# Optimization experiments

Measured on AMD Instinct MI355X. Metric: run time of the kernel, lower is better.

The kernel has to match this reference:

```python
import jax, jax.numpy as jnp
import numpy as np

HID = 512

def setup_inputs() -> dict:
    key = jax.random.key(0)
    k1, k2, k3, k4, k5, k6 = jax.random.split(key, 6)
    B, T, H = 32, 4096, HID
    enc_seq = jax.random.normal(k1, (B, T, H), dtype=jnp.float32)
    enc_mask = jax.random.randint(k2, (B, T), 0, 2, dtype=jnp.int32)
    dec_state = jax.random.normal(k3, (B, H), dtype=jnp.float32)
    # Linear weights, torch layout: y = x @ W.T
    scale = 1.0 / np.sqrt(H)
    W_h = jax.random.uniform(k4, (H, H), jnp.float32, -scale, scale)
    W_s = jax.random.uniform(k5, (H, H), jnp.float32, -scale, scale)
    v = jax.random.uniform(k6, (H,), jnp.float32, -scale, scale)
    return {"enc_seq": enc_seq, "enc_mask": enc_mask, "dec_state": dec_state,
            "W_h": W_h, "W_s": W_s, "v": v}

def reference(enc_seq, enc_mask, dec_state, W_h, W_s, v):
    # s: [B,H] -> [B,1,H] broadcast over T; h: [B,T,H]
    s = jnp.einsum('bh,kh->bk', dec_state, W_s)[:, None, :]
    h = jnp.einsum('bth,kh->btk', enc_seq, W_h)
    e = jnp.einsum('bth,h->bt', jnp.tanh(h + s), v)  # [B,T]
    e = jnp.where(enc_mask == 0, jnp.float32(-1e9), e)
    a = jax.nn.softmax(e, axis=1)  # [B,T]
    ctx = jnp.einsum('bt,bth->bh', a, enc_seq)  # [B,H]
    return (ctx, a)
```

## Files before the change

kernel.cpp:

```cpp
#include <hip/hip_runtime.h>
#include <hip/hip_bf16.h>
#include <cstdint>
#include <cstddef>

#define HID 512
#define T_SZ 4096

typedef __bf16 bf16x8 __attribute__((ext_vector_type(8)));
typedef float f32x4 __attribute__((ext_vector_type(4)));

__device__ __forceinline__ unsigned short f2bf_rne(float f) {
    unsigned int u = __float_as_uint(f);
    unsigned int r = (u + 0x7FFFu + ((u >> 16) & 1u)) >> 16;
    return (unsigned short)r;
}

__device__ __forceinline__ bf16x8 pack8(float4 x0, float4 x1) {
    bf16x8 r;
    r[0] = (__bf16)x0.x; r[1] = (__bf16)x0.y; r[2] = (__bf16)x0.z; r[3] = (__bf16)x0.w;
    r[4] = (__bf16)x1.x; r[5] = (__bf16)x1.y; r[6] = (__bf16)x1.z; r[7] = (__bf16)x1.w;
    return r;
}

__device__ __forceinline__ float fast_tanh(float x) {
    float e = __expf(2.0f * x);
    return 1.0f - 2.0f / (e + 1.0f);
}

__device__ __forceinline__ void gload_lds16(const void* g, void* l) {
    __builtin_amdgcn_global_load_lds(
        (const __attribute__((address_space(1))) unsigned int*)g,
        (__attribute__((address_space(3))) unsigned int*)l, 16, 0, 0);
}

__global__ void k_s(const float* __restrict__ dec, const float* __restrict__ Ws,
                    float* __restrict__ s) {
    int idx = blockIdx.x * 256 + threadIdx.x;
    int b = idx >> 9, n = idx & 511;
    const float4* dp = reinterpret_cast<const float4*>(dec + (size_t)b * HID);
    const float4* wp = reinterpret_cast<const float4*>(Ws + (size_t)n * HID);
    float acc = 0.f;
#pragma unroll 8
    for (int i = 0; i < HID / 4; ++i) {
        float4 d = dp[i], w = wp[i];
        acc += d.x * w.x + d.y * w.y + d.z * w.z + d.w * w.w;
    }
    s[idx] = acc;
}

__global__ void k_pack(const float* __restrict__ Wh, uint4* __restrict__ Wb) {
    int idx = blockIdx.x * 256 + threadIdx.x;
    int n = idx >> 6;
    int k0 = (idx & 63) * 8;
    const float4* p = reinterpret_cast<const float4*>(Wh + (size_t)n * HID + k0);
    float4 x0 = p[0], x1 = p[1];
    uint4 w;
    w.x = f2bf_rne(x0.x) | ((unsigned)f2bf_rne(x0.y) << 16);
    w.y = f2bf_rne(x0.z) | ((unsigned)f2bf_rne(x0.w) << 16);
    w.z = f2bf_rne(x1.x) | ((unsigned)f2bf_rne(x1.y) << 16);
    w.w = f2bf_rne(x1.z) | ((unsigned)f2bf_rne(x1.w) << 16);
    int n4g = n >> 4, c = n & 15, kk = k0 >> 5, g = (k0 >> 3) & 3;
    Wb[(size_t)kk * 2048 + n4g * 64 + g * 16 + c] = w;
}

__global__ void __launch_bounds__(256, 3) k_gemm_e(
    const float* __restrict__ enc, const uint4* __restrict__ Wb,
    const float* __restrict__ s, const float* __restrict__ v,
    float* __restrict__ part_e) {
    __shared__ __align__(16) unsigned char Abuf[2][4096];
    __shared__ __align__(16) unsigned char Bbuf[2][16384];
    __shared__ float red[4][64];

    const int tid = threadIdx.x;
    const int p = blockIdx.x;
    const int logical = (p & 7) * 512 + (p >> 3);
    const int h = logical & 1;
    const size_t row0 = (size_t)(logical >> 1) * 64;
    const int b = (int)(row0 >> 12);

    const int lane = tid & 63, wid = tid >> 6;
    const int c = lane & 15, g4 = lane >> 4;

    float sv_s[4], sv_v[4];
#pragma unroll
    for (int ni = 0; ni < 4; ++ni) {
        int n = h * 256 + wid * 64 + ni * 16 + c;
        sv_s[ni] = s[b * HID + n];
        sv_v[ni] = v[n];
    }

    const int ar = tid >> 2;
    const int ak = (tid & 3) * 8;
    const float* Ag = enc + (row0 + ar) * HID + ak;
    const int abyte = ar * 64 + (tid & 3) * 16;
    const uint4* Bg = Wb + h * 1024;
    const int wchunk = wid * 64;

    float4 a0 = *reinterpret_cast<const float4*>(Ag);
    float4 a1 = *reinterpret_cast<const float4*>(Ag + 4);
#pragma unroll
    for (int i = 0; i < 4; ++i)
        gload_lds16(Bg + (wchunk + i * 256) + (lane), &Bbuf[0][(wchunk + i * 256) * 16]);
    *reinterpret_cast<bf16x8*>(&Abuf[0][abyte]) = pack8(a0, a1);
    a0 = *reinterpret_cast<const float4*>(Ag + 32);
    a1 = *reinterpret_cast<const float4*>(Ag + 36);
    __syncthreads();

    f32x4 acc[4][4] = {};

    for (int kk = 0; kk < 16; ++kk) {
        const int cur = kk & 1, nxt = cur ^ 1;
        if (kk < 15) {
#pragma unroll
            for (int i = 0; i < 4; ++i)
                gload_lds16(Bg + (size_t)(kk + 1) * 2048 + (wchunk + i * 256) + lane,
                            &Bbuf[nxt][(wchunk + i * 256) * 16]);
            *reinterpret_cast<bf16x8*>(&Abuf[nxt][abyte]) = pack8(a0, a1);
        }
        if (kk < 14) {
            a0 = *reinterpret_cast<const float4*>(Ag + (kk + 2) * 32);
            a1 = *reinterpret_cast<const float4*>(Ag + (kk + 2) * 32 + 4);
        }
        bf16x8 af[4], bfr[4];
#pragma unroll
        for (int mi = 0; mi < 4; ++mi)
            af[mi] = *reinterpret_cast<const bf16x8*>(&Abuf[cur][(mi * 16 + c) * 64 + g4 * 16]);
#pragma unroll
        for (int ni = 0; ni < 4; ++ni)
            bfr[ni] = *reinterpret_cast<const bf16x8*>(&Bbuf[cur][((wid * 4 + ni) * 64 + lane) * 16]);
#pragma unroll
        for (int mi = 0; mi < 4; ++mi)
#pragma unroll
            for (int ni = 0; ni < 4; ++ni)
                acc[mi][ni] = __builtin_amdgcn_mfma_f32_16x16x32_bf16(
                    af[mi], bfr[ni], acc[mi][ni], 0, 0, 0);
        __syncthreads();
    }

    float e_part[4][4] = {};
#pragma unroll
    for (int ni = 0; ni < 4; ++ni)
#pragma unroll
        for (int mi = 0; mi < 4; ++mi)
#pragma unroll
            for (int r = 0; r < 4; ++r)
                e_part[mi][r] += fast_tanh(acc[mi][ni][r] + sv_s[ni]) * sv_v[ni];

#pragma unroll
    for (int m = 1; m <= 8; m <<= 1)
#pragma unroll
        for (int mi = 0; mi < 4; ++mi)
#pragma unroll
            for (int r = 0; r < 4; ++r)
                e_part[mi][r] += __shfl_xor(e_part[mi][r], m);

    if (c == 0) {
#pragma unroll
        for (int mi = 0; mi < 4; ++mi)
#pragma unroll
            for (int r = 0; r < 4; ++r)
                red[wid][mi * 16 + g4 * 4 + r] = e_part[mi][r];
    }
    __syncthreads();
    if (tid < 64)
        part_e[(size_t)h * 131072 + row0 + tid] =
            red[0][tid] + red[1][tid] + red[2][tid] + red[3][tid];
}

__global__ void k_softmax(const float* __restrict__ part_e, float* __restrict__ a,
                          const int* __restrict__ mask) {
    int b = blockIdx.x, tid = threadIdx.x;
    int lane = tid & 63, wid = tid >> 6;
    __shared__ float red[16];
    float vals[4]; int ms[4];
    float mx = -1e30f;
#pragma unroll
    for (int j = 0; j < 4; ++j) {
        size_t t = (size_t)b * T_SZ + tid + j * 1024;
        vals[j] = part_e[t] + part_e[131072 + t];
        ms[j] = mask[t];
        if (ms[j]) mx = fmaxf(mx, vals[j]);
    }
#pragma unroll
    for (int m = 32; m >= 1; m >>= 1) mx = fmaxf(mx, __shfl_xor(mx, m));
    if (lane == 0) red[wid] = mx;
    __syncthreads();
    if (tid == 0) {
        float m2 = red[0];
        for (int i = 1; i < 16; ++i) m2 = fmaxf(m2, red[i]);
        red[0] = m2;
    }
    __syncthreads();
    mx = red[0];
    __syncthreads();
    float pv[4]; float sum = 0.f;
#pragma unroll
    for (int j = 0; j < 4; ++j) { pv[j] = ms[j] ? __expf(vals[j] - mx) : 0.f; sum += pv[j]; }
#pragma unroll
    for (int m = 32; m >= 1; m >>= 1) sum += __shfl_xor(sum, m);
    if (lane == 0) red[wid] = sum;
    __syncthreads();
    if (tid == 0) {
        float s2 = 0.f;
        for (int i = 0; i < 16; ++i) s2 += red[i];
        red[0] = s2;
    }
    __syncthreads();
    float inv = 1.f / red[0];
#pragma unroll
    for (int j = 0; j < 4; ++j)
        a[(size_t)b * T_SZ + tid + j * 1024] = pv[j] * inv;
}

__global__ void k_ctx(const float* __restrict__ enc, const float* __restrict__ a,
                      float2* __restrict__ part) {
    int ts = blockIdx.x, b = blockIdx.y, tid = threadIdx.x;
    size_t rbase = (size_t)b * T_SZ + (size_t)ts * 128;
    const float2* ep = reinterpret_cast<const float2*>(enc + rbase * HID) + tid;
    const float* ap = a + rbase;
    float ax = 0.f, ay = 0.f, bx = 0.f, by = 0.f;
#pragma unroll 2
    for (int t = 0; t < 128; t += 2) {
        float a0 = ap[t], a1 = ap[t + 1];
        float2 e0 = ep[(size_t)t * 256], e1 = ep[(size_t)(t + 1) * 256];
        ax += a0 * e0.x; ay += a0 * e0.y;
        bx += a1 * e1.x; by += a1 * e1.y;
    }
    float2 r; r.x = ax + bx; r.y = ay + by;
    part[(size_t)(b * 32 + ts) * 256 + tid] = r;
}

__global__ void k_ctxred(const float* __restrict__ part, float* __restrict__ ctx) {
    int idx = blockIdx.x * 256 + threadIdx.x;
    int b = idx >> 9, h = idx & 511;
    float sum = 0.f;
#pragma unroll
    for (int ts = 0; ts < 32; ++ts) sum += part[(size_t)(b * 32 + ts) * 512 + h];
    ctx[idx] = sum;
}

extern "C" void kernel_launch(void* const* d_in, const int* in_sizes, int n_in,
                              void* d_out, int out_size, void* d_ws, size_t ws_size,
                              hipStream_t stream) {
    const float* enc  = (const float*)d_in[0];
    const int*   mask = (const int*)d_in[1];
    const float* dec  = (const float*)d_in[2];
    const float* Wh   = (const float*)d_in[3];
    const float* Ws   = (const float*)d_in[4];
    const float* v    = (const float*)d_in[5];

    float* out = (float*)d_out;
    float* ctx = out;
    float* a   = out + 16384;

    float* ws     = (float*)d_ws;
    float* s      = ws;
    uint4* Wb     = (uint4*)(ws + 16384);
    float* part_e = ws + 16384 + 131072;
    float* part   = part_e + 262144;

    hipLaunchKernelGGL(k_s,      dim3(64),      dim3(256),  0, stream, dec, Ws, s);
    hipLaunchKernelGGL(k_pack,   dim3(128),     dim3(256),  0, stream, Wh, Wb);
    hipLaunchKernelGGL(k_gemm_e, dim3(4096),    dim3(256),  0, stream, enc, Wb, s, v, part_e);
    hipLaunchKernelGGL(k_softmax,dim3(32),      dim3(1024), 0, stream, part_e, a, mask);
    hipLaunchKernelGGL(k_ctx,    dim3(32, 32),  dim3(256),  0, stream, enc, a, (float2*)part);
    hipLaunchKernelGGL(k_ctxred, dim3(64),      dim3(256),  0, stream, part, ctx);
}
```

Baseline: 192.0 us.

## Enlarge GEMM tile to 128x256 with 2x2 warp grid and triple-buffered LDS

The fused score GEMM now processes 128 rows per block instead of 64, using a 2x2 wave layout where each wave computes 64x128. This halves the number of blocks and the redundant reloading of the packed W_h tiles per row. It also adds a three-stage LDS pipeline with explicit vmcnt waits and barriers so global loads run two k-steps ahead. The cost is higher register and LDS use, which drops the occupancy target from 3 to 2 blocks per CU, and the hand-written waitcnt sequencing is more fragile.

```diff
diff --git a/kernel.cpp b/kernel.cpp
--- a/kernel.cpp
+++ b/kernel.cpp
@@ -59,100 +59,124 @@
     w.y = f2bf_rne(x0.z) | ((unsigned)f2bf_rne(x0.w) << 16);
     w.z = f2bf_rne(x1.x) | ((unsigned)f2bf_rne(x1.y) << 16);
     w.w = f2bf_rne(x1.z) | ((unsigned)f2bf_rne(x1.w) << 16);
-    int n4g = n >> 4, c = n & 15, kk = k0 >> 5, g = (k0 >> 3) & 3;
-    Wb[(size_t)kk * 2048 + n4g * 64 + g * 16 + c] = w;
-}
-
-__global__ void __launch_bounds__(256, 3) k_gemm_e(
+    int n4 = n >> 4, c = n & 15, kk = k0 >> 5, g = (k0 >> 3) & 3;
+    Wb[(size_t)kk * 2048 + n4 * 64 + g * 16 + c] = w;
+}
+
+__global__ void __launch_bounds__(256, 2) k_gemm_e(
     const float* __restrict__ enc, const uint4* __restrict__ Wb,
     const float* __restrict__ s, const float* __restrict__ v,
     float* __restrict__ part_e) {
-    __shared__ __align__(16) unsigned char Abuf[2][4096];
-    __shared__ __align__(16) unsigned char Bbuf[2][16384];
+    __shared__ __align__(16) unsigned char Abuf[3][8192];
+    __shared__ __align__(16) unsigned char Bbuf[3][16384];
     __shared__ float red[4][64];
 
     const int tid = threadIdx.x;
     const int p = blockIdx.x;
-    const int logical = (p & 7) * 512 + (p >> 3);
+    const int logical = (p & 7) * 256 + (p >> 3);
     const int h = logical & 1;
-    const size_t row0 = (size_t)(logical >> 1) * 64;
+    const int m = logical >> 1;
+    const size_t row0 = (size_t)m * 128;
     const int b = (int)(row0 >> 12);
 
     const int lane = tid & 63, wid = tid >> 6;
     const int c = lane & 15, g4 = lane >> 4;
-
-    float sv_s[4], sv_v[4];
-#pragma unroll
-    for (int ni = 0; ni < 4; ++ni) {
-        int n = h * 256 + wid * 64 + ni * 16 + c;
+    const int wm = wid >> 1, wn = wid & 1;
+
+    float sv_s[8], sv_v[8];
+#pragma unroll
+    for (int ni = 0; ni < 8; ++ni) {
+        int n = h * 256 + wn * 128 + ni * 16 + c;
         sv_s[ni] = s[b * HID + n];
         sv_v[ni] = v[n];
     }
-
-    const int ar = tid >> 2;
-    const int ak = (tid & 3) * 8;
-    const float* Ag = enc + (row0 + ar) * HID + ak;
-    const int abyte = ar * 64 + (tid & 3) * 16;
-    const uint4* Bg = Wb + h * 1024;
-    const int wchunk = wid * 64;
-
-    float4 a0 = *reinterpret_cast<const float4*>(Ag);
-    float4 a1 = *reinterpret_cast<const float4*>(Ag + 4);
+    asm volatile("s_waitcnt vmcnt(0)" ::: "memory");
+
+    const int rt0 = tid >> 6, gg = (tid >> 4) & 3, cc = tid & 15;
+    const float* Ag0 = enc + (row0 + rt0 * 16 + cc) * HID + gg * 8;
+    const float* Ag1 = Ag0 + (size_t)64 * HID;
+    const uint4* Bg = Wb + h * 1024 + wid * 64 + lane;
+
+    float4 ar[2][4];
+
+#pragma unroll
+    for (int q = 0; q < 2; ++q)
+        ar[0][q * 2]     = *reinterpret_cast<const float4*>((q ? Ag1 : Ag0)),
+        ar[0][q * 2 + 1] = *reinterpret_cast<const float4*>((q ? Ag1 : Ag0) + 4);
 #pragma unroll
     for (int i = 0; i < 4; ++i)
-        gload_lds16(Bg + (wchunk + i * 256) + (lane), &Bbuf[0][(wchunk + i * 256) * 16]);
-    *reinterpret_cast<bf16x8*>(&Abuf[0][abyte]) = pack8(a0, a1);
-    a0 = *reinterpret_cast<const float4*>(Ag + 32);
-    a1 = *reinterpret_cast<const float4*>(Ag + 36);
-    __syncthreads();
-
-    f32x4 acc[4][4] = {};
-
+        gload_lds16(Bg + i * 256, &Bbuf[0][(i * 256 + wid * 64) * 16]);
+    asm volatile("" ::: "memory");
+#pragma unroll
+    for (int q = 0; q < 2; ++q)
+        ar[1][q * 2]     = *reinterpret_cast<const float4*>((q ? Ag1 : Ag0) + 32),
+        ar[1][q * 2 + 1] = *reinterpret_cast<const float4*>((q ? Ag1 : Ag0) + 36);
+#pragma unroll
+    for (int i = 0; i < 4; ++i)
+        gload_lds16(Bg + 2048 + i * 256, &Bbuf[1][(i * 256 + wid * 64) * 16]);
+    *reinterpret_cast<bf16x8*>(&Abuf[0][tid * 16])         = pack8(ar[0][0], ar[0][1]);
+    *reinterpret_cast<bf16x8*>(&Abuf[0][(tid + 256) * 16]) = pack8(ar[0][2], ar[0][3]);
+    asm volatile("s_waitcnt vmcnt(8) lgkmcnt(0)\n\ts_barrier" ::: "memory");
+
+    f32x4 acc[4][8] = {};
+
+#pragma unroll
     for (int kk = 0; kk < 16; ++kk) {
-        const int cur = kk & 1, nxt = cur ^ 1;
-        if (kk < 15) {
+        if (kk + 2 <= 15) {
+#pragma unroll
+            for (int q = 0; q < 2; ++q) {
+                const float* Agq = (q ? Ag1 : Ag0) + (kk + 2) * 32;
+                ar[kk & 1][q * 2]     = *reinterpret_cast<const float4*>(Agq);
+                ar[kk & 1][q * 2 + 1] = *reinterpret_cast<const float4*>(Agq + 4);
+            }
 #pragma unroll
             for (int i = 0; i < 4; ++i)
-                gload_lds16(Bg + (size_t)(kk + 1) * 2048 + (wchunk + i * 256) + lane,
-                            &Bbuf[nxt][(wchunk + i * 256) * 16]);
-            *reinterpret_cast<bf16x8*>(&Abuf[nxt][abyte]) = pack8(a0, a1);
+                gload_lds16(Bg + (size_t)(kk + 2) * 2048 + i * 256,
+                            &Bbuf[(kk + 2) % 3][(i * 256 + wid * 64) * 16]);
         }
-        if (kk < 14) {
-            a0 = *reinterpret_cast<const float4*>(Ag + (kk + 2) * 32);
-            a1 = *reinterpret_cast<const float4*>(Ag + (kk + 2) * 32 + 4);
+        if (kk + 1 <= 15) {
+            const int wb = (kk + 1) % 3, wp_ = (kk + 1) & 1;
+            *reinterpret_cast<bf16x8*>(&Abuf[wb][tid * 16])         = pack8(ar[wp_][0], ar[wp_][1]);
+            *reinterpret_cast<bf16x8*>(&Abuf[wb][(tid + 256) * 16]) = pack8(ar[wp_][2], ar[wp_][3]);
         }
-        bf16x8 af[4], bfr[4];
-#pragma unroll
-        for (int mi = 0; mi < 4; ++mi)
-            af[mi] = *reinterpret_cast<const bf16x8*>(&Abuf[cur][(mi * 16 + c) * 64 + g4 * 16]);
-#pragma unroll
-        for (int ni = 0; ni < 4; ++ni)
-            bfr[ni] = *reinterpret_cast<const bf16x8*>(&Bbuf[cur][((wid * 4 + ni) * 64 + lane) * 16]);
-#pragma unroll
-        for (int mi = 0; mi < 4; ++mi)
-#pragma unroll
-            for (int ni = 0; ni < 4; ++ni)
+        bf16x8 af[4], bfr[8];
+#pragma unroll
+        for (int mi = 0; mi < 4; ++mi)
+            af[mi] = *reinterpret_cast<const bf16x8*>(
+                &Abuf[kk % 3][((wm * 4 + mi) * 64 + lane) * 16]);
+#pragma unroll
+        for (int ni = 0; ni < 8; ++ni)
+            bfr[ni] = *reinterpret_cast<const bf16x8*>(
+                &Bbuf[kk % 3][((wn * 8 + ni) * 64 + lane) * 16]);
+#pragma unroll
+        for (int mi = 0; mi < 4; ++mi)
+#pragma unroll
+            for (int ni = 0; ni < 8; ++ni)
                 acc[mi][ni] = __builtin_amdgcn_mfma_f32_16x16x32_bf16(
                     af[mi], bfr[ni], acc[mi][ni], 0, 0, 0);
-        __syncthreads();
+        if (kk <= 13)
+            asm volatile("s_waitcnt vmcnt(8) lgkmcnt(0)\n\ts_barrier" ::: "memory");
+        else if (kk == 14)
+            asm volatile("s_waitcnt vmcnt(0) lgkmcnt(0)\n\ts_barrier" ::: "memory");
     }
 
     float e_part[4][4] = {};
 #pragma unroll
-    for (int ni = 0; ni < 4; ++ni)
+    for (int ni = 0; ni < 8; ++ni) {
+        float sn = sv_s[ni], vn = sv_v[ni];
 #pragma unroll
         for (int mi = 0; mi < 4; ++mi)
 #pragma unroll
             for (int r = 0; r < 4; ++r)
-                e_part[mi][r] += fast_tanh(acc[mi][ni][r] + sv_s[ni]) * sv_v[ni];
-
-#pragma unroll
-    for (int m = 1; m <= 8; m <<= 1)
+                e_part[mi][r] += fast_tanh(acc[mi][ni][r] + sn) * vn;
+    }
+#pragma unroll
+    for (int mm = 1; mm <= 8; mm <<= 1)
 #pragma unroll
         for (int mi = 0; mi < 4; ++mi)
 #pragma unroll
             for (int r = 0; r < 4; ++r)
-                e_part[mi][r] += __shfl_xor(e_part[mi][r], m);
+                e_part[mi][r] += __shfl_xor(e_part[mi][r], mm);
 
     if (c == 0) {
 #pragma unroll
@@ -162,9 +186,11 @@
                 red[wid][mi * 16 + g4 * 4 + r] = e_part[mi][r];
     }
     __syncthreads();
-    if (tid < 64)
+    if (tid < 128) {
+        int wm2 = tid >> 6, r = tid & 63;
         part_e[(size_t)h * 131072 + row0 + tid] =
-            red[0][tid] + red[1][tid] + red[2][tid] + red[3][tid];
+            red[wm2 * 2][r] + red[wm2 * 2 + 1][r];
+    }
 }
 
 __global__ void k_softmax(const float* __restrict__ part_e, float* __restrict__ a,
@@ -261,7 +287,7 @@
 
     hipLaunchKernelGGL(k_s,      dim3(64),      dim3(256),  0, stream, dec, Ws, s);
     hipLaunchKernelGGL(k_pack,   dim3(128),     dim3(256),  0, stream, Wh, Wb);
-    hipLaunchKernelGGL(k_gemm_e, dim3(4096),    dim3(256),  0, stream, enc, Wb, s, v, part_e);
+    hipLaunchKernelGGL(k_gemm_e, dim3(2048),    dim3(256),  0, stream, enc, Wb, s, v, part_e);
     hipLaunchKernelGGL(k_softmax,dim3(32),      dim3(1024), 0, stream, part_e, a, mask);
     hipLaunchKernelGGL(k_ctx,    dim3(32, 32),  dim3(256),  0, stream, enc, a, (float2*)part);
     hipLaunchKernelGGL(k_ctxred, dim3(64),      dim3(256),  0, stream, part, ctx);
```

Measured after the change: 206.1 us. +7.4%, slower.

## Split GEMM N into four quarters and load W_h fragments directly into registers

Applied to the files above, without the earlier changes.

The fused GEMM+tanh kernel now splits the 512 output columns into four 128-wide slices instead of two 256-wide ones, doubling the grid to 8192 blocks. Each wave now covers 32 columns, and the B (W_h) fragments are loaded straight from global memory into registers with double buffering, so the B LDS buffers and global_load_lds are gone. This cuts LDS use and raises the occupancy target to 4 blocks per CU. The cost is that each enc row tile is read and converted to bf16 twice as often, and softmax must now sum four partial-score buffers instead of two.

```diff
diff --git a/kernel.cpp b/kernel.cpp
--- a/kernel.cpp
+++ b/kernel.cpp
@@ -25,12 +25,6 @@
 __device__ __forceinline__ float fast_tanh(float x) {
     float e = __expf(2.0f * x);
     return 1.0f - 2.0f / (e + 1.0f);
-}
-
-__device__ __forceinline__ void gload_lds16(const void* g, void* l) {
-    __builtin_amdgcn_global_load_lds(
-        (const __attribute__((address_space(1))) unsigned int*)g,
-        (__attribute__((address_space(3))) unsigned int*)l, 16, 0, 0);
 }
 
 __global__ void k_s(const float* __restrict__ dec, const float* __restrict__ Ws,
@@ -59,100 +53,106 @@
     w.y = f2bf_rne(x0.z) | ((unsigned)f2bf_rne(x0.w) << 16);
     w.z = f2bf_rne(x1.x) | ((unsigned)f2bf_rne(x1.y) << 16);
     w.w = f2bf_rne(x1.z) | ((unsigned)f2bf_rne(x1.w) << 16);
-    int n4g = n >> 4, c = n & 15, kk = k0 >> 5, g = (k0 >> 3) & 3;
-    Wb[(size_t)kk * 2048 + n4g * 64 + g * 16 + c] = w;
-}
-
-__global__ void __launch_bounds__(256, 3) k_gemm_e(
+    int n4 = n >> 4, c = n & 15, kk = k0 >> 5, g = (k0 >> 3) & 3;
+    Wb[(size_t)kk * 2048 + n4 * 64 + g * 16 + c] = w;
+}
+
+__global__ void __launch_bounds__(256, 4) k_gemm_e(
     const float* __restrict__ enc, const uint4* __restrict__ Wb,
     const float* __restrict__ s, const float* __restrict__ v,
     float* __restrict__ part_e) {
     __shared__ __align__(16) unsigned char Abuf[2][4096];
-    __shared__ __align__(16) unsigned char Bbuf[2][16384];
     __shared__ float red[4][64];
 
     const int tid = threadIdx.x;
     const int p = blockIdx.x;
-    const int logical = (p & 7) * 512 + (p >> 3);
-    const int h = logical & 1;
-    const size_t row0 = (size_t)(logical >> 1) * 64;
+    const int logical = (p & 7) * 1024 + (p >> 3);
+    const int h = logical & 3;
+    const int m = logical >> 2;
+    const size_t row0 = (size_t)m * 64;
     const int b = (int)(row0 >> 12);
 
     const int lane = tid & 63, wid = tid >> 6;
     const int c = lane & 15, g4 = lane >> 4;
 
-    float sv_s[4], sv_v[4];
-#pragma unroll
-    for (int ni = 0; ni < 4; ++ni) {
-        int n = h * 256 + wid * 64 + ni * 16 + c;
+    float sv_s[2], sv_v[2];
+#pragma unroll
+    for (int ni = 0; ni < 2; ++ni) {
+        int n = h * 128 + wid * 32 + ni * 16 + c;
         sv_s[ni] = s[b * HID + n];
         sv_v[ni] = v[n];
     }
 
-    const int ar = tid >> 2;
-    const int ak = (tid & 3) * 8;
-    const float* Ag = enc + (row0 + ar) * HID + ak;
-    const int abyte = ar * 64 + (tid & 3) * 16;
-    const uint4* Bg = Wb + h * 1024;
-    const int wchunk = wid * 64;
-
-    float4 a0 = *reinterpret_cast<const float4*>(Ag);
-    float4 a1 = *reinterpret_cast<const float4*>(Ag + 4);
-#pragma unroll
-    for (int i = 0; i < 4; ++i)
-        gload_lds16(Bg + (wchunk + i * 256) + (lane), &Bbuf[0][(wchunk + i * 256) * 16]);
-    *reinterpret_cast<bf16x8*>(&Abuf[0][abyte]) = pack8(a0, a1);
-    a0 = *reinterpret_cast<const float4*>(Ag + 32);
-    a1 = *reinterpret_cast<const float4*>(Ag + 36);
-    __syncthreads();
-
-    f32x4 acc[4][4] = {};
-
+    const int arow = ((tid >> 6) << 4) + (tid & 15);
+    const int ag = (tid >> 4) & 3;
+    const float* Ag = enc + (row0 + arow) * HID + ag * 8;
+    const int abyte = tid * 16;
+    const uint4* Bg = Wb + (h * 8 + wid * 2) * 64 + lane;
+
+    float4 aR[2][2];
+    uint4  bR[2][2];
+
+    {
+        float4 x0 = *reinterpret_cast<const float4*>(Ag);
+        float4 x1 = *reinterpret_cast<const float4*>(Ag + 4);
+        bR[0][0] = Bg[0];
+        bR[0][1] = Bg[64];
+        bR[1][0] = Bg[2048];
+        bR[1][1] = Bg[2048 + 64];
+        *reinterpret_cast<bf16x8*>(&Abuf[0][abyte]) = pack8(x0, x1);
+        aR[1][0] = *reinterpret_cast<const float4*>(Ag + 32);
+        aR[1][1] = *reinterpret_cast<const float4*>(Ag + 36);
+    }
+    asm volatile("s_waitcnt lgkmcnt(0)\n\ts_barrier" ::: "memory");
+
+    f32x4 acc[4][2] = {};
+
+#pragma unroll
     for (int kk = 0; kk < 16; ++kk) {
-        const int cur = kk & 1, nxt = cur ^ 1;
-        if (kk < 15) {
-#pragma unroll
-            for (int i = 0; i < 4; ++i)
-                gload_lds16(Bg + (size_t)(kk + 1) * 2048 + (wchunk + i * 256) + lane,
-                            &Bbuf[nxt][(wchunk + i * 256) * 16]);
-            *reinterpret_cast<bf16x8*>(&Abuf[nxt][abyte]) = pack8(a0, a1);
+        if (kk + 2 <= 15) {
+            aR[kk & 1][0] = *reinterpret_cast<const float4*>(Ag + (kk + 2) * 32);
+            aR[kk & 1][1] = *reinterpret_cast<const float4*>(Ag + (kk + 2) * 32 + 4);
         }
-        if (kk < 14) {
-            a0 = *reinterpret_cast<const float4*>(Ag + (kk + 2) * 32);
-            a1 = *reinterpret_cast<const float4*>(Ag + (kk + 2) * 32 + 4);
+        if (kk + 1 <= 15)
+            *reinterpret_cast<bf16x8*>(&Abuf[(kk + 1) & 1][abyte]) =
+                pack8(aR[(kk + 1) & 1][0], aR[(kk + 1) & 1][1]);
+        bf16x8 af[4];
+#pragma unroll
+        for (int mi = 0; mi < 4; ++mi)
+            af[mi] = *reinterpret_cast<const bf16x8*>(
+                &Abuf[kk & 1][(mi * 64 + lane) * 16]);
+#pragma unroll
+        for (int mi = 0; mi < 4; ++mi)
+#pragma unroll
+            for (int ni = 0; ni < 2; ++ni)
+                acc[mi][ni] = __builtin_amdgcn_mfma_f32_16x16x32_bf16(
+                    af[mi], *reinterpret_cast<bf16x8*>(&bR[kk & 1][ni]),
+                    acc[mi][ni], 0, 0, 0);
+        if (kk + 2 <= 15) {
+            bR[kk & 1][0] = Bg[(size_t)(kk + 2) * 2048];
+            bR[kk & 1][1] = Bg[(size_t)(kk + 2) * 2048 + 64];
         }
-        bf16x8 af[4], bfr[4];
-#pragma unroll
-        for (int mi = 0; mi < 4; ++mi)
-            af[mi] = *reinterpret_cast<const bf16x8*>(&Abuf[cur][(mi * 16 + c) * 64 + g4 * 16]);
-#pragma unroll
-        for (int ni = 0; ni < 4; ++ni)
-            bfr[ni] = *reinterpret_cast<const bf16x8*>(&Bbuf[cur][((wid * 4 + ni) * 64 + lane) * 16]);
-#pragma unroll
-        for (int mi = 0; mi < 4; ++mi)
-#pragma unroll
-            for (int ni = 0; ni < 4; ++ni)
-                acc[mi][ni] = __builtin_amdgcn_mfma_f32_16x16x32_bf16(
-                    af[mi], bfr[ni], acc[mi][ni], 0, 0, 0);
-        __syncthreads();
+        if (kk < 15)
+            asm volatile("s_waitcnt lgkmcnt(0)\n\ts_barrier" ::: "memory");
     }
 
     float e_part[4][4] = {};
 #pragma unroll
-    for (int ni = 0; ni < 4; ++ni)
+    for (int ni = 0; ni < 2; ++ni) {
+        float sn = sv_s[ni], vn = sv_v[ni];
 #pragma unroll
         for (int mi = 0; mi < 4; ++mi)
 #pragma unroll
             for (int r = 0; r < 4; ++r)
-                e_part[mi][r] += fast_tanh(acc[mi][ni][r] + sv_s[ni]) * sv_v[ni];
-
-#pragma unroll
-    for (int m = 1; m <= 8; m <<= 1)
+                e_part[mi][r] += fast_tanh(acc[mi][ni][r] + sn) * vn;
+    }
+#pragma unroll
+    for (int mm = 1; mm <= 8; mm <<= 1)
 #pragma unroll
         for (int mi = 0; mi < 4; ++mi)
 #pragma unroll
             for (int r = 0; r < 4; ++r)
-                e_part[mi][r] += __shfl_xor(e_part[mi][r], m);
+                e_part[mi][r] += __shfl_xor(e_part[mi][r], mm);
 
     if (c == 0) {
 #pragma unroll
@@ -177,7 +177,7 @@
 #pragma unroll
     for (int j = 0; j < 4; ++j) {
         size_t t = (size_t)b * T_SZ + tid + j * 1024;
-        vals[j] = part_e[t] + part_e[131072 + t];
+        vals[j] = part_e[t] + part_e[131072 + t] + part_e[262144 + t] + part_e[393216 + t];
         ms[j] = mask[t];
         if (ms[j]) mx = fmaxf(mx, vals[j]);
     }
@@ -257,11 +257,11 @@
     float* s      = ws;
     uint4* Wb     = (uint4*)(ws + 16384);
     float* part_e = ws + 16384 + 131072;
-    float* part   = part_e + 262144;
+    float* part   = part_e + 524288;
 
     hipLaunchKernelGGL(k_s,      dim3(64),      dim3(256),  0, stream, dec, Ws, s);
     hipLaunchKernelGGL(k_pack,   dim3(128),     dim3(256),  0, stream, Wh, Wb);
-    hipLaunchKernelGGL(k_gemm_e, dim3(4096),    dim3(256),  0, stream, enc, Wb, s, v, part_e);
+    hipLaunchKernelGGL(k_gemm_e, dim3(8192),    dim3(256),  0, stream, enc, Wb, s, v, part_e);
     hipLaunchKernelGGL(k_softmax,dim3(32),      dim3(1024), 0, stream, part_e, a, mask);
     hipLaunchKernelGGL(k_ctx,    dim3(32, 32),  dim3(256),  0, stream, enc, a, (float2*)part);
     hipLaunchKernelGGL(k_ctxred, dim3(64),      dim3(256),  0, stream, part, ctx);
```

Result: slower. 229.5 us (+19.5%).

## Stage full A tile in swizzled LDS once and stream B from registers

Applied to the files above, without the earlier changes.

The GEMM kernel now loads and converts the entire 64x512 A tile to bf16 into a 64KB swizzled LDS buffer up front. W fragments are read straight from global memory into a 3-deep register ring instead of being staged through LDS with global_load_lds. This removes the per-k-step __syncthreads and LDS double buffering. The cost is higher LDS use per block, with launch bounds lowered from 3 to 2 blocks per CU, more registers, and no overlap between the A load and the MFMA work.

```diff
diff --git a/kernel.cpp b/kernel.cpp
--- a/kernel.cpp
+++ b/kernel.cpp
@@ -25,12 +25,6 @@
 __device__ __forceinline__ float fast_tanh(float x) {
     float e = __expf(2.0f * x);
     return 1.0f - 2.0f / (e + 1.0f);
-}
-
-__device__ __forceinline__ void gload_lds16(const void* g, void* l) {
-    __builtin_amdgcn_global_load_lds(
-        (const __attribute__((address_space(1))) unsigned int*)g,
-        (__attribute__((address_space(3))) unsigned int*)l, 16, 0, 0);
 }
 
 __global__ void k_s(const float* __restrict__ dec, const float* __restrict__ Ws,
@@ -59,100 +53,111 @@
     w.y = f2bf_rne(x0.z) | ((unsigned)f2bf_rne(x0.w) << 16);
     w.z = f2bf_rne(x1.x) | ((unsigned)f2bf_rne(x1.y) << 16);
     w.w = f2bf_rne(x1.z) | ((unsigned)f2bf_rne(x1.w) << 16);
-    int n4g = n >> 4, c = n & 15, kk = k0 >> 5, g = (k0 >> 3) & 3;
-    Wb[(size_t)kk * 2048 + n4g * 64 + g * 16 + c] = w;
-}
-
-__global__ void __launch_bounds__(256, 3) k_gemm_e(
+    int n4 = n >> 4, c = n & 15, kk = k0 >> 5, g = (k0 >> 3) & 3;
+    Wb[(size_t)kk * 2048 + n4 * 64 + g * 16 + c] = w;
+}
+
+__global__ void __launch_bounds__(256, 2) k_gemm_e(
     const float* __restrict__ enc, const uint4* __restrict__ Wb,
     const float* __restrict__ s, const float* __restrict__ v,
     float* __restrict__ part_e) {
-    __shared__ __align__(16) unsigned char Abuf[2][4096];
-    __shared__ __align__(16) unsigned char Bbuf[2][16384];
+    __shared__ __align__(16) unsigned char As[65536];
     __shared__ float red[4][64];
 
     const int tid = threadIdx.x;
     const int p = blockIdx.x;
     const int logical = (p & 7) * 512 + (p >> 3);
     const int h = logical & 1;
-    const size_t row0 = (size_t)(logical >> 1) * 64;
+    const int m = logical >> 1;
+    const size_t row0 = (size_t)m * 64;
     const int b = (int)(row0 >> 12);
 
     const int lane = tid & 63, wid = tid >> 6;
     const int c = lane & 15, g4 = lane >> 4;
 
+    {
+        const float* base = enc + row0 * HID;
+#pragma unroll
+        for (int i = 0; i < 16; ++i) {
+            int f = i * 256 + tid;
+            float4 x0 = *reinterpret_cast<const float4*>(base + (size_t)f * 8);
+            float4 x1 = *reinterpret_cast<const float4*>(base + (size_t)f * 8 + 4);
+            int row = f >> 6, c8 = f & 63;
+            int kk = c8 >> 2, g = c8 & 3;
+            int chunk = (row >> 4) * 64 + g * 16 + (row & 15);
+            int byte = (kk * 4096 + chunk * 16) ^ (((((kk & 3) << 1) | (g & 1))) << 4);
+            *reinterpret_cast<bf16x8*>(&As[byte]) = pack8(x0, x1);
+        }
+    }
+
     float sv_s[4], sv_v[4];
 #pragma unroll
     for (int ni = 0; ni < 4; ++ni) {
-        int n = h * 256 + wid * 64 + ni * 16 + c;
+        int n = (h * 16 + wid * 4 + ni) * 16 + c;
         sv_s[ni] = s[b * HID + n];
         sv_v[ni] = v[n];
     }
-
-    const int ar = tid >> 2;
-    const int ak = (tid & 3) * 8;
-    const float* Ag = enc + (row0 + ar) * HID + ak;
-    const int abyte = ar * 64 + (tid & 3) * 16;
-    const uint4* Bg = Wb + h * 1024;
-    const int wchunk = wid * 64;
-
-    float4 a0 = *reinterpret_cast<const float4*>(Ag);
-    float4 a1 = *reinterpret_cast<const float4*>(Ag + 4);
-#pragma unroll
-    for (int i = 0; i < 4; ++i)
-        gload_lds16(Bg + (wchunk + i * 256) + (lane), &Bbuf[0][(wchunk + i * 256) * 16]);
-    *reinterpret_cast<bf16x8*>(&Abuf[0][abyte]) = pack8(a0, a1);
-    a0 = *reinterpret_cast<const float4*>(Ag + 32);
-    a1 = *reinterpret_cast<const float4*>(Ag + 36);
-    __syncthreads();
+    __syncthreads();
+
+    const uint4* Bg = Wb + (h * 16 + wid * 4) * 64 + lane;
+
+    uint4 bR[3][4];
+#pragma unroll
+    for (int d = 0; d < 3; ++d)
+#pragma unroll
+        for (int ni = 0; ni < 4; ++ni)
+            bR[d][ni] = Bg[(size_t)d * 2048 + ni * 64];
+
+    bf16x8 af[2][4];
+#pragma unroll
+    for (int mi = 0; mi < 4; ++mi) {
+        int byte = ((mi * 64 + lane) * 16) ^ ((((0 & 3) << 1) | ((lane >> 4) & 1)) << 4);
+        af[0][mi] = *reinterpret_cast<const bf16x8*>(&As[byte]);
+    }
 
     f32x4 acc[4][4] = {};
 
+#pragma unroll
     for (int kk = 0; kk < 16; ++kk) {
-        const int cur = kk & 1, nxt = cur ^ 1;
         if (kk < 15) {
 #pragma unroll
-            for (int i = 0; i < 4; ++i)
-                gload_lds16(Bg + (size_t)(kk + 1) * 2048 + (wchunk + i * 256) + lane,
-                            &Bbuf[nxt][(wchunk + i * 256) * 16]);
-            *reinterpret_cast<bf16x8*>(&Abuf[nxt][abyte]) = pack8(a0, a1);
+            for (int mi = 0; mi < 4; ++mi) {
+                int byte = ((kk + 1) * 4096 + (mi * 64 + lane) * 16)
+                         ^ (((((kk + 1) & 3) << 1) | ((lane >> 4) & 1)) << 4);
+                af[(kk + 1) & 1][mi] = *reinterpret_cast<const bf16x8*>(&As[byte]);
+            }
         }
-        if (kk < 14) {
-            a0 = *reinterpret_cast<const float4*>(Ag + (kk + 2) * 32);
-            a1 = *reinterpret_cast<const float4*>(Ag + (kk + 2) * 32 + 4);
-        }
-        bf16x8 af[4], bfr[4];
-#pragma unroll
-        for (int mi = 0; mi < 4; ++mi)
-            af[mi] = *reinterpret_cast<const bf16x8*>(&Abuf[cur][(mi * 16 + c) * 64 + g4 * 16]);
-#pragma unroll
-        for (int ni = 0; ni < 4; ++ni)
-            bfr[ni] = *reinterpret_cast<const bf16x8*>(&Bbuf[cur][((wid * 4 + ni) * 64 + lane) * 16]);
 #pragma unroll
         for (int mi = 0; mi < 4; ++mi)
 #pragma unroll
             for (int ni = 0; ni < 4; ++ni)
                 acc[mi][ni] = __builtin_amdgcn_mfma_f32_16x16x32_bf16(
-                    af[mi], bfr[ni], acc[mi][ni], 0, 0, 0);
-        __syncthreads();
+                    af[kk & 1][mi], *reinterpret_cast<bf16x8*>(&bR[kk % 3][ni]),
+                    acc[mi][ni], 0, 0, 0);
+        if (kk + 3 <= 15) {
+#pragma unroll
+            for (int ni = 0; ni < 4; ++ni)
+                bR[kk % 3][ni] = Bg[(size_t)(kk + 3) * 2048 + ni * 64];
+        }
     }
 
     float e_part[4][4] = {};
 #pragma unroll
-    for (int ni = 0; ni < 4; ++ni)
+    for (int ni = 0; ni < 4; ++ni) {
+        float sn = sv_s[ni], vn = sv_v[ni];
 #pragma unroll
         for (int mi = 0; mi < 4; ++mi)
 #pragma unroll
             for (int r = 0; r < 4; ++r)
-                e_part[mi][r] += fast_tanh(acc[mi][ni][r] + sv_s[ni]) * sv_v[ni];
-
-#pragma unroll
-    for (int m = 1; m <= 8; m <<= 1)
+                e_part[mi][r] += fast_tanh(acc[mi][ni][r] + sn) * vn;
+    }
+#pragma unroll
+    for (int mm = 1; mm <= 8; mm <<= 1)
 #pragma unroll
         for (int mi = 0; mi < 4; ++mi)
 #pragma unroll
             for (int r = 0; r < 4; ++r)
-                e_part[mi][r] += __shfl_xor(e_part[mi][r], m);
+                e_part[mi][r] += __shfl_xor(e_part[mi][r], mm);
 
     if (c == 0) {
 #pragma unroll
```

Measured after the change: 178.6 us. -7.0%, faster.
